# Kernel tuning notes

Hardware: AMD Instinct MI355X
Metric: run time of the kernel (lower is better)

Reference implementation:

```python
import jax, jax.numpy as jnp
import numpy as np

ROUTINGS = 3
EPS = 1e-9

def _squash(s):
    # squash along the capsule-vector (last) axis
    sq = jnp.sum(s * s, axis=-1, keepdims=True)
    return s * (sq / (1.0 + sq)) / jnp.sqrt(sq + EPS)

def setup_inputs() -> dict:
    key = jax.random.key(0)
    k1, k2 = jax.random.split(key)
    B, N, D, d = 32, 64, 128, 128  # batch, num_capsule(=input_num_capsule), dim_capsule, input_dim_capsule
    x = jax.random.normal(k1, (B, N, d), dtype=jnp.float32)
    W = jax.random.normal(k2, (1, N, N, D, d), dtype=jnp.float32)
    return {"x": x, "W": W}

def reference(x, W):
    # u[b,j,k,:] = W[0,j,k] @ x[b,j]  (faithful to broadcast matmul, N==I)
    u = jnp.einsum('jkde,bje->bjkd', W[0], x)  # (B,N,N,D)
    b = jnp.zeros_like(u)                      # routing logits carry D axis per source
    v = None
    for i in range(ROUTINGS):
        c = jax.nn.softmax(b, axis=2)
        s = jnp.sum(c * u, axis=1, keepdims=True)  # (B,1,N,D)
        v = _squash(s)
        if i < ROUTINGS - 1:
            b = b + u * v  # (inputs*outputs).sum over trailing singleton dim
    return v[:, 0, :, :, None]  # (B,N,D,1) matching torch outputs.squeeze(1)
```

## Files before the change

### kernel.cpp

```cpp
#include <hip/hip_runtime.h>

#define NB 32
#define NN 64
#define ND 128
#define NE 128
#define NK 64

typedef float  f32x4  __attribute__((ext_vector_type(4)));
typedef short  short8 __attribute__((ext_vector_type(8)));
typedef __bf16 bf16x8 __attribute__((ext_vector_type(8)));

union Frag { bf16x8 h; short8 s; };

static constexpr size_t U_BYTES = (size_t)NB * NN * ND * NK * 2;
static constexpr size_t V_BYTES = (size_t)NB * ND * NK * 4;
static constexpr size_t WS_NEED = U_BYTES + 2 * V_BYTES;

#define GLOAD16(g, l)                                                   \
    __builtin_amdgcn_global_load_lds(                                   \
        (const __attribute__((address_space(1))) void*)(g),             \
        (__attribute__((address_space(3))) void*)(l), 16, 0, 0)

template <int CTRL, int RMASK>
__device__ __forceinline__ float dppf(float x) {
    int xi = __float_as_int(x);
    return __int_as_float(__builtin_amdgcn_update_dpp(xi, xi, CTRL, RMASK, 0xF, false));
}
__device__ __forceinline__ float wave_sum(float x) {
    x += dppf<0xB1, 0xF>(x);
    x += dppf<0x4E, 0xF>(x);
    x += dppf<0x141, 0xF>(x);
    x += dppf<0x140, 0xF>(x);
    x += dppf<0x142, 0xA>(x);
    x += dppf<0x143, 0xC>(x);
    return __int_as_float(__builtin_amdgcn_readlane(__float_as_int(x), 63));
}

__device__ __forceinline__ ushort f2bf(float f) {
    __bf16 h = (__bf16)f;
    ushort r;
    __builtin_memcpy(&r, &h, 2);
    return r;
}
__device__ __forceinline__ float bf2f(ushort r) {
    return __int_as_float(((int)r) << 16);
}
__device__ __forceinline__ void cvt8(const float4& a, const float4& b, Frag& fr) {
    fr.h[0] = (__bf16)a.x; fr.h[1] = (__bf16)a.y; fr.h[2] = (__bf16)a.z; fr.h[3] = (__bf16)a.w;
    fr.h[4] = (__bf16)b.x; fr.h[5] = (__bf16)b.y; fr.h[6] = (__bf16)b.z; fr.h[7] = (__bf16)b.w;
}

__global__ __launch_bounds__(256, 3) void k_u(const float* __restrict__ W,
                                              const float* __restrict__ x,
                                              ushort* __restrict__ u) {
    __shared__ float  Wl[4][2][1024];
    __shared__ ushort T[4][32][72];
    const int t  = threadIdx.x;
    const int wv = t >> 6;
    const int l  = t & 63;
    const int gw = blockIdx.x * 4 + wv;
    const int j  = gw >> 7;
    const int d  = gw & 127;

    const int lr = l & 15;
    const int lh = l >> 4;
    const int e0 = lh * 8;

    const float* xb = x + (size_t)j * NE;
    float4 xf[2][4][2];
#pragma unroll
    for (int mt = 0; mt < 2; ++mt)
#pragma unroll
        for (int ec = 0; ec < 4; ++ec) {
            const float* p = xb + (size_t)(mt * 16 + lr) * (NN * NE) + ec * 32 + e0;
            xf[mt][ec][0] = *reinterpret_cast<const float4*>(p);
            xf[mt][ec][1] = *reinterpret_cast<const float4*>(p + 4);
        }
    asm volatile("s_waitcnt vmcnt(0)" ::: "memory");
    __builtin_amdgcn_sched_barrier(0);
    Frag a[2][4];
#pragma unroll
    for (int mt = 0; mt < 2; ++mt)
#pragma unroll
        for (int ec = 0; ec < 4; ++ec) cvt8(xf[mt][ec][0], xf[mt][ec][1], a[mt][ec]);

    const char* Wg = (const char*)W + ((size_t)(j * NN) * ND + d) * (NE * 4);
#define STAGE(c, buf)                                                       \
    {                                                                       \
        const int nt_ = (c) >> 1, eh_ = (c) & 1;                            \
        const char* gp_ = Wg + (size_t)(nt_ * 16 + lr) * 65536 + eh_ * 256; \
        _Pragma("unroll") for (int i_ = 0; i_ < 4; ++i_)                    \
            GLOAD16(gp_ + (i_ * 4 + lh) * 16, &Wl[wv][buf][i_ * 256]);      \
    }

    STAGE(0, 0);
    STAGE(1, 1);

    f32x4 acc[2][4];
#pragma unroll
    for (int mt = 0; mt < 2; ++mt)
#pragma unroll
        for (int nt = 0; nt < 4; ++nt) acc[mt][nt] = (f32x4)0.0f;

#pragma unroll
    for (int c = 0; c < 8; ++c) {
        const int nt = c >> 1, eh = c & 1, buf = c & 1;
        if (c < 7) { asm volatile("s_waitcnt vmcnt(4)" ::: "memory"); }
        else       { asm volatile("s_waitcnt vmcnt(0)" ::: "memory"); }
        __builtin_amdgcn_sched_barrier(0);

        const float* cb = &Wl[wv][buf][0];
        f32x4 g[2][2];
#pragma unroll
        for (int ec = 0; ec < 2; ++ec) {
            const int sl = (ec * 8 + lh * 2) * 64 + lr * 4;
            g[ec][0] = *reinterpret_cast<const f32x4*>(cb + sl);
            g[ec][1] = *reinterpret_cast<const f32x4*>(cb + sl + 64);
        }
        asm volatile("s_waitcnt lgkmcnt(0)" ::: "memory");
        __builtin_amdgcn_sched_barrier(0);
        if (c < 6) STAGE(c + 2, buf);

#pragma unroll
        for (int ec = 0; ec < 2; ++ec) {
            Frag bw;
            float4 f0 = {g[ec][0][0], g[ec][0][1], g[ec][0][2], g[ec][0][3]};
            float4 f1 = {g[ec][1][0], g[ec][1][1], g[ec][1][2], g[ec][1][3]};
            cvt8(f0, f1, bw);
#pragma unroll
            for (int mt = 0; mt < 2; ++mt)
                acc[mt][nt] = __builtin_amdgcn_mfma_f32_16x16x32_bf16(
                    a[mt][eh * 2 + ec].s, bw.s, acc[mt][nt], 0, 0, 0);
        }
    }
#undef STAGE

#pragma unroll
    for (int mt = 0; mt < 2; ++mt)
#pragma unroll
        for (int nt = 0; nt < 4; ++nt)
#pragma unroll
            for (int r = 0; r < 4; ++r)
                T[wv][mt * 16 + lh * 4 + r][nt * 16 + lr] = f2bf(acc[mt][nt][r]);
    __syncthreads();

    const int b2 = l >> 1;
    const int kh = (l & 1) * 32;
    ushort* up = u + (((size_t)b2 * NN + j) * ND + d) * NK + kh;
    const ushort* tp = &T[wv][b2][kh];
#pragma unroll
    for (int i = 0; i < 4; ++i) {
        short8 v = *reinterpret_cast<const short8*>(tp + i * 8);
        *reinterpret_cast<short8*>(up + i * 8) = v;
    }
}

__global__ __launch_bounds__(512) void k_route(const ushort* __restrict__ u,
                                               const float* __restrict__ Vsum,
                                               float* __restrict__ s,
                                               int first) {
    __shared__ float P[8][8][65];
    const int b  = blockIdx.x >> 4;
    const int dg = blockIdx.x & 15;
    const int t  = threadIdx.x;
    const int wv = t >> 6;
    const int l  = t & 63;

    float sacc[8];
#pragma unroll
    for (int dd = 0; dd < 8; ++dd) sacc[dd] = 0.0f;

    const ushort* ub = u + (((size_t)b * NN + wv * 8) * ND + dg * 8) * NK + l;

    if (first) {
        for (int jj = 0; jj < 8; ++jj) {
            const ushort* up = ub + (size_t)jj * (ND * NK);
#pragma unroll
            for (int dd = 0; dd < 8; ++dd) sacc[dd] += bf2f(up[dd * NK]);
        }
#pragma unroll
        for (int dd = 0; dd < 8; ++dd) sacc[dd] *= (1.0f / 64.0f);
    } else {
        float vs[8];
#pragma unroll
        for (int dd = 0; dd < 8; ++dd)
            vs[dd] = Vsum[((size_t)b * ND + dg * 8 + dd) * NK + l];

        for (int jj = 0; jj < 8; ++jj) {
            const ushort* up = ub + (size_t)jj * (ND * NK);
            float uv[8];
#pragma unroll
            for (int dd = 0; dd < 8; ++dd) uv[dd] = bf2f(up[dd * NK]);
#pragma unroll
            for (int dd = 0; dd < 8; ++dd) {
                float p = __expf(uv[dd] * vs[dd] - 32.0f);
                float q = wave_sum(p);
                sacc[dd] = fmaf(p * __builtin_amdgcn_rcpf(q), uv[dd], sacc[dd]);
            }
        }
    }

#pragma unroll
    for (int dd = 0; dd < 8; ++dd) P[wv][dd][l] = sacc[dd];
    __syncthreads();

    const int dd = t >> 6;
    const int k  = t & 63;
    float r = P[0][dd][k];
#pragma unroll
    for (int w2 = 1; w2 < 8; ++w2) r += P[w2][dd][k];
    s[((size_t)b * ND + dg * 8 + dd) * NK + k] = r;
}

__global__ __launch_bounds__(256) void k_squash(const float* __restrict__ s,
                                                float* __restrict__ Vsum,
                                                float* __restrict__ out,
                                                int mode) {
    const int t  = threadIdx.x;
    const int gw = blockIdx.x * 4 + (t >> 6);
    const int b  = gw >> 6;
    const int k  = gw & 63;
    const int l  = t & 63;

    const float s0 = s[((size_t)b * ND + l) * NK + k];
    const float s1 = s[((size_t)b * ND + l + 64) * NK + k];
    float sq    = wave_sum(fmaf(s0, s0, s1 * s1));
    float scale = (sq / (1.0f + sq)) * rsqrtf(sq + 1e-9f);
    float v0 = s0 * scale, v1 = s1 * scale;
    if (mode == 2) {
        float* op = out + ((size_t)b * NN + k) * ND;
        op[l]      = v0;
        op[l + 64] = v1;
    } else if (mode == 0) {
        float* vp = Vsum + (size_t)b * ND * NK + k;
        vp[(size_t)l * NK]        = v0;
        vp[(size_t)(l + 64) * NK] = v1;
    } else {
        float* vp = Vsum + (size_t)b * ND * NK + k;
        vp[(size_t)l * NK]        += v0;
        vp[(size_t)(l + 64) * NK] += v1;
    }
}

extern "C" void kernel_launch(void* const* d_in, const int* in_sizes, int n_in,
                              void* d_out, int out_size, void* d_ws, size_t ws_size,
                              hipStream_t stream) {
    (void)in_sizes; (void)n_in; (void)out_size;
    const float* x = (const float*)d_in[0];
    const float* W = (const float*)d_in[1];
    float* out = (float*)d_out;

    if (ws_size < WS_NEED) return;
    char* ws = (char*)d_ws;
    ushort* u   = (ushort*)ws;
    float* Vsum = (float*)(ws + U_BYTES);
    float* s    = (float*)(ws + U_BYTES + V_BYTES);

    k_u<<<dim3(2048), dim3(256), 0, stream>>>(W, x, u);
    for (int it = 0; it < 3; ++it) {
        k_route<<<dim3(512), dim3(512), 0, stream>>>(u, Vsum, s, it == 0 ? 1 : 0);
        k_squash<<<dim3(512), dim3(256), 0, stream>>>(s, Vsum, out, it);
    }
}
```

Measured before the change: 123.3 us.

## Compute two d rows per wave in k_u with swizzled larger W staging

Each wave now handles two adjacent d indices, so the bf16 x fragments held in registers are reused across twice as much W, and the grid shrinks to 1024 blocks. W is staged in full 16-row by 2-d chunks per n-tile using an XOR-swizzled LDS layout to avoid bank conflicts. The staging buffer and the output transpose tile now share LDS through a union, and the block-wide __syncthreads is replaced by per-wave waitcnts. Per-wave LDS grows to 32KB and launch bounds drop to 1 block, which lowers occupancy and raises register pressure.

```diff
diff --git a/kernel.cpp b/kernel.cpp
--- a/kernel.cpp
+++ b/kernel.cpp
@@ -50,21 +50,28 @@
     fr.h[4] = (__bf16)b.x; fr.h[5] = (__bf16)b.y; fr.h[6] = (__bf16)b.z; fr.h[7] = (__bf16)b.w;
 }
 
-__global__ __launch_bounds__(256, 3) void k_u(const float* __restrict__ W,
+__global__ __launch_bounds__(256, 1) void k_u(const float* __restrict__ W,
                                               const float* __restrict__ x,
                                               ushort* __restrict__ u) {
-    __shared__ float  Wl[4][2][1024];
-    __shared__ ushort T[4][32][72];
+    struct WaveSh {
+        union {
+            float  w[2][4096];
+            ushort t[2][32][72];
+        };
+    };
+    __shared__ WaveSh sh[4];
+
     const int t  = threadIdx.x;
     const int wv = t >> 6;
     const int l  = t & 63;
     const int gw = blockIdx.x * 4 + wv;
-    const int j  = gw >> 7;
-    const int d  = gw & 127;
+    const int j  = gw >> 6;
+    const int dp = gw & 63;
+    const int d0 = dp * 2;
 
     const int lr = l & 15;
     const int lh = l >> 4;
-    const int e0 = lh * 8;
+    const int sx = lr & 7;
 
     const float* xb = x + (size_t)j * NE;
     float4 xf[2][4][2];
@@ -72,7 +79,7 @@
     for (int mt = 0; mt < 2; ++mt)
 #pragma unroll
         for (int ec = 0; ec < 4; ++ec) {
-            const float* p = xb + (size_t)(mt * 16 + lr) * (NN * NE) + ec * 32 + e0;
+            const float* p = xb + (size_t)(mt * 16 + lr) * (NN * NE) + ec * 32 + lh * 8;
             xf[mt][ec][0] = *reinterpret_cast<const float4*>(p);
             xf[mt][ec][1] = *reinterpret_cast<const float4*>(p + 4);
         }
@@ -84,74 +91,92 @@
 #pragma unroll
         for (int ec = 0; ec < 4; ++ec) cvt8(xf[mt][ec][0], xf[mt][ec][1], a[mt][ec]);
 
-    const char* Wg = (const char*)W + ((size_t)(j * NN) * ND + d) * (NE * 4);
-#define STAGE(c, buf)                                                       \
-    {                                                                       \
-        const int nt_ = (c) >> 1, eh_ = (c) & 1;                            \
-        const char* gp_ = Wg + (size_t)(nt_ * 16 + lr) * 65536 + eh_ * 256; \
-        _Pragma("unroll") for (int i_ = 0; i_ < 4; ++i_)                    \
-            GLOAD16(gp_ + (i_ * 4 + lh) * 16, &Wl[wv][buf][i_ * 256]);      \
+    const char* Wg = (const char*)W + (((size_t)(j * NN)) * ND + d0) * (NE * 4);
+#define STAGE(nt, buf)                                                        \
+    {                                                                         \
+        _Pragma("unroll") for (int kk = 0; kk < 16; ++kk) {                   \
+            const char* gp_ = Wg + (size_t)((nt) * 16 + kk) * 65536 +         \
+                              ((l ^ (kk & 7)) * 16);                          \
+            GLOAD16(gp_, &sh[wv].w[buf][kk * 256]);                           \
+        }                                                                     \
     }
 
     STAGE(0, 0);
     STAGE(1, 1);
 
-    f32x4 acc[2][4];
-#pragma unroll
-    for (int mt = 0; mt < 2; ++mt)
-#pragma unroll
-        for (int nt = 0; nt < 4; ++nt) acc[mt][nt] = (f32x4)0.0f;
-
-#pragma unroll
-    for (int c = 0; c < 8; ++c) {
-        const int nt = c >> 1, eh = c & 1, buf = c & 1;
-        if (c < 7) { asm volatile("s_waitcnt vmcnt(4)" ::: "memory"); }
-        else       { asm volatile("s_waitcnt vmcnt(0)" ::: "memory"); }
+    f32x4 acc[2][2][4];
+#pragma unroll
+    for (int dd = 0; dd < 2; ++dd)
+#pragma unroll
+        for (int mt = 0; mt < 2; ++mt)
+#pragma unroll
+            for (int nt = 0; nt < 4; ++nt) acc[dd][mt][nt] = (f32x4)0.0f;
+
+#pragma unroll
+    for (int nt = 0; nt < 4; ++nt) {
+        const int buf = nt & 1;
+        if (nt < 3) { asm volatile("s_waitcnt vmcnt(16)" ::: "memory"); }
+        else        { asm volatile("s_waitcnt vmcnt(0)" ::: "memory"); }
         __builtin_amdgcn_sched_barrier(0);
 
-        const float* cb = &Wl[wv][buf][0];
-        f32x4 g[2][2];
-#pragma unroll
-        for (int ec = 0; ec < 2; ++ec) {
-            const int sl = (ec * 8 + lh * 2) * 64 + lr * 4;
-            g[ec][0] = *reinterpret_cast<const f32x4*>(cb + sl);
-            g[ec][1] = *reinterpret_cast<const f32x4*>(cb + sl + 64);
-        }
+        const char* cb = (const char*)&sh[wv].w[buf][0] + lr * 1024;
+        f32x4 g[2][4][2];
+#pragma unroll
+        for (int dd = 0; dd < 2; ++dd)
+#pragma unroll
+            for (int ec = 0; ec < 4; ++ec)
+#pragma unroll
+                for (int h = 0; h < 2; ++h) {
+                    const int pos = (dd * 32 + ec * 8 + lh * 2 + h) ^ sx;
+                    g[dd][ec][h] = *reinterpret_cast<const f32x4*>(cb + pos * 16);
+                }
         asm volatile("s_waitcnt lgkmcnt(0)" ::: "memory");
         __builtin_amdgcn_sched_barrier(0);
-        if (c < 6) STAGE(c + 2, buf);
-
-#pragma unroll
-        for (int ec = 0; ec < 2; ++ec) {
-            Frag bw;
-            float4 f0 = {g[ec][0][0], g[ec][0][1], g[ec][0][2], g[ec][0][3]};
-            float4 f1 = {g[ec][1][0], g[ec][1][1], g[ec][1][2], g[ec][1][3]};
-            cvt8(f0, f1, bw);
-#pragma unroll
-            for (int mt = 0; mt < 2; ++mt)
-                acc[mt][nt] = __builtin_amdgcn_mfma_f32_16x16x32_bf16(
-                    a[mt][eh * 2 + ec].s, bw.s, acc[mt][nt], 0, 0, 0);
-        }
+        if (nt < 2) STAGE(nt + 2, buf);
+
+#pragma unroll
+        for (int dd = 0; dd < 2; ++dd)
+#pragma unroll
+            for (int ec = 0; ec < 4; ++ec) {
+                Frag bw;
+                float4 f0 = {g[dd][ec][0][0], g[dd][ec][0][1], g[dd][ec][0][2], g[dd][ec][0][3]};
+                float4 f1 = {g[dd][ec][1][0], g[dd][ec][1][1], g[dd][ec][1][2], g[dd][ec][1][3]};
+                cvt8(f0, f1, bw);
+#pragma unroll
+                for (int mt = 0; mt < 2; ++mt)
+                    acc[dd][mt][nt] = __builtin_amdgcn_mfma_f32_16x16x32_bf16(
+                        a[mt][ec].s, bw.s, acc[dd][mt][nt], 0, 0, 0);
+            }
     }
 #undef STAGE
 
-#pragma unroll
-    for (int mt = 0; mt < 2; ++mt)
-#pragma unroll
-        for (int nt = 0; nt < 4; ++nt)
-#pragma unroll
-            for (int r = 0; r < 4; ++r)
-                T[wv][mt * 16 + lh * 4 + r][nt * 16 + lr] = f2bf(acc[mt][nt][r]);
-    __syncthreads();
+    asm volatile("s_waitcnt lgkmcnt(0)" ::: "memory");
+    __builtin_amdgcn_sched_barrier(0);
+
+#pragma unroll
+    for (int dd = 0; dd < 2; ++dd)
+#pragma unroll
+        for (int mt = 0; mt < 2; ++mt)
+#pragma unroll
+            for (int nt = 0; nt < 4; ++nt)
+#pragma unroll
+                for (int r = 0; r < 4; ++r)
+                    sh[wv].t[dd][mt * 16 + lh * 4 + r][nt * 16 + lr] =
+                        f2bf(acc[dd][mt][nt][r]);
+    asm volatile("s_waitcnt lgkmcnt(0)" ::: "memory");
+    __builtin_amdgcn_sched_barrier(0);
 
     const int b2 = l >> 1;
     const int kh = (l & 1) * 32;
-    ushort* up = u + (((size_t)b2 * NN + j) * ND + d) * NK + kh;
-    const ushort* tp = &T[wv][b2][kh];
-#pragma unroll
-    for (int i = 0; i < 4; ++i) {
-        short8 v = *reinterpret_cast<const short8*>(tp + i * 8);
-        *reinterpret_cast<short8*>(up + i * 8) = v;
+#pragma unroll
+    for (int dd = 0; dd < 2; ++dd) {
+        ushort* up = u + (((size_t)b2 * NN + j) * ND + (d0 + dd)) * NK + kh;
+        const ushort* tp = &sh[wv].t[dd][b2][kh];
+#pragma unroll
+        for (int i = 0; i < 4; ++i) {
+            short8 v = *reinterpret_cast<const short8*>(tp + i * 8);
+            *reinterpret_cast<short8*>(up + i * 8) = v;
+        }
     }
 }
 
@@ -256,7 +281,7 @@
     float* Vsum = (float*)(ws + U_BYTES);
     float* s    = (float*)(ws + U_BYTES + V_BYTES);
 
-    k_u<<<dim3(2048), dim3(256), 0, stream>>>(W, x, u);
+    k_u<<<dim3(1024), dim3(256), 0, stream>>>(W, x, u);
     for (int it = 0; it < 3; ++it) {
         k_route<<<dim3(512), dim3(512), 0, stream>>>(u, Vsum, s, it == 0 ? 1 : 0);
         k_squash<<<dim3(512), dim3(256), 0, stream>>>(s, Vsum, out, it);
```

Result: slower. 130.7 us (+6.0%).
